# Performance work log

Hardware: AMD Instinct MI355X
Metric: run time of the kernel (lower is better)

Reference implementation:

```python
import jax, jax.numpy as jnp
import numpy as np

B, S, D, H = 2, 2048, 1024, 16
DK = D // H


def setup_inputs() -> dict:
    key = jax.random.key(0)
    ks = jax.random.split(key, 13)
    std = 1.0 / np.sqrt(D)
    inp = {
        "query": jax.random.normal(ks[0], (B, S, D), jnp.float32),
        "key": jax.random.normal(ks[1], (B, S, D), jnp.float32),
        "value": jax.random.normal(ks[2], (B, S, D), jnp.float32),
        "mask": jax.random.randint(ks[3], (B, S, S), 0, 2, jnp.int32),
        "Wq": jax.random.normal(ks[4], (D, D), jnp.float32) * std,
        "bq": jax.random.normal(ks[5], (D,), jnp.float32) * std,
        "Wk": jax.random.normal(ks[6], (D, D), jnp.float32) * std,
        "bk": jax.random.normal(ks[7], (D,), jnp.float32) * std,
        "Wv": jax.random.normal(ks[8], (D, D), jnp.float32) * std,
        "bv": jax.random.normal(ks[9], (D,), jnp.float32) * std,
        "Wo": jax.random.normal(ks[10], (D, D), jnp.float32) * std,
        "bo": jax.random.normal(ks[11], (D,), jnp.float32) * std,
    }
    return inp


def reference(query, key, value, mask, Wq, bq, Wk, bk, Wv, bv, Wo, bo):
    # QKV projections (torch Linear: x @ W.T + b), then split heads -> [B,H,S,DK]
    def proj(x, W, b):
        return (x @ W.T + b).reshape(B, S, H, DK).transpose(0, 2, 1, 3)

    q = proj(query, Wq, bq)
    k = proj(key, Wk, bk)
    v = proj(value, Wv, bv)

    scores = jnp.einsum("bhqd,bhkd->bhqk", q, k) / np.sqrt(DK)
    # mask [B,S,S] broadcast over heads; masked_fill(mask==0, -1e9)
    scores = jnp.where(mask[:, None, :, :] == 0, jnp.float32(-1e9), scores)
    p_attn = jax.nn.softmax(scores, axis=-1)
    x = jnp.einsum("bhqk,bhkd->bhqd", p_attn, v)
    x = x.transpose(0, 2, 1, 3).reshape(B, S, D)
    return x @ Wo.T + bo
```

## Files before the change

### kernel.cpp

```cpp
#include <hip/hip_runtime.h>
#include <hip/hip_bf16.h>
#include <cstdint>
#include <cstddef>

#define NB 2
#define NS 2048
#define ND 1024
#define NH 16
#define NDK 64
#define NT (NS / 64)

typedef __attribute__((ext_vector_type(4))) float f32x4;
typedef __attribute__((ext_vector_type(8))) short bf16x8;

#define MFMA_16x16x32_BF16(a,b,c) __builtin_amdgcn_mfma_f32_16x16x32_bf16((a),(b),(c),0,0,0)

__device__ __forceinline__ uint16_t f2bf(float f){
  uint32_t u = __float_as_uint(f);
  u += 0x7fffu + ((u >> 16) & 1u);
  return (uint16_t)(u >> 16);
}
__device__ __forceinline__ uint32_t bfpack2(float a, float b){
  uint32_t r;
  asm volatile("v_cvt_pk_bf16_f32 %0, %1, %2" : "=v"(r) : "v"(a), "v"(b));
  return r;
}
__device__ __forceinline__ void gload_lds16(const void* g, void* l){
  __builtin_amdgcn_global_load_lds((const __attribute__((address_space(1))) void*)g,
                                   (__attribute__((address_space(3))) void*)l, 16, 0, 0);
}

__global__ void prep_inputs(const float* __restrict__ a, const float* __restrict__ b2,
                            const float* __restrict__ c, uint16_t* __restrict__ oa,
                            uint16_t* __restrict__ ob, uint16_t* __restrict__ oc,
                            const int* __restrict__ mask, unsigned long long* __restrict__ bits,
                            int n8, int nchunks){
  if(blockIdx.y == 3){
    int wid  = (blockIdx.x * blockDim.x + threadIdx.x) >> 6;
    int lane = threadIdx.x & 63;
    int nw   = (gridDim.x * blockDim.x) >> 6;
    for(int ch = wid; ch < nchunks; ch += nw){
      int mv = mask[(size_t)ch * 64 + lane];
      unsigned long long bb = __ballot(mv != 0);
      if(lane == 0) bits[ch] = bb;
    }
    return;
  }
  const float* in = (blockIdx.y == 0) ? a : (blockIdx.y == 1) ? b2 : c;
  uint16_t* out   = (blockIdx.y == 0) ? oa : (blockIdx.y == 1) ? ob : oc;
  int i0 = blockIdx.x * blockDim.x + threadIdx.x;
  int stride = gridDim.x * blockDim.x;
  for(int i = i0; i < n8; i += stride){
    const float4* p = (const float4*)(in) + (size_t)i * 2;
    float4 x = p[0], y = p[1];
    bf16x8 o;
    o[0]=(short)f2bf(x.x); o[1]=(short)f2bf(x.y); o[2]=(short)f2bf(x.z); o[3]=(short)f2bf(x.w);
    o[4]=(short)f2bf(y.x); o[5]=(short)f2bf(y.y); o[6]=(short)f2bf(y.z); o[7]=(short)f2bf(y.w);
    *((bf16x8*)(out) + i) = o;
  }
}
__global__ void cvt4_f32_bf16(const float* __restrict__ a, const float* __restrict__ b2,
                              const float* __restrict__ c, const float* __restrict__ d,
                              uint16_t* __restrict__ oa, uint16_t* __restrict__ ob,
                              uint16_t* __restrict__ oc, uint16_t* __restrict__ od, int n8){
  const float* in = (blockIdx.y == 0) ? a : (blockIdx.y == 1) ? b2 : (blockIdx.y == 2) ? c : d;
  uint16_t* out   = (blockIdx.y == 0) ? oa : (blockIdx.y == 1) ? ob : (blockIdx.y == 2) ? oc : od;
  int i0 = blockIdx.x * blockDim.x + threadIdx.x;
  int stride = gridDim.x * blockDim.x;
  for(int i = i0; i < n8; i += stride){
    const float4* p = (const float4*)(in) + (size_t)i * 2;
    float4 x = p[0], y = p[1];
    bf16x8 o;
    o[0]=(short)f2bf(x.x); o[1]=(short)f2bf(x.y); o[2]=(short)f2bf(x.z); o[3]=(short)f2bf(x.w);
    o[4]=(short)f2bf(y.x); o[5]=(short)f2bf(y.y); o[6]=(short)f2bf(y.z); o[7]=(short)f2bf(y.w);
    *((bf16x8*)(out) + i) = o;
  }
}

template<bool OUTF32>
__global__ __launch_bounds__(256, 4)
void gemm_bt(const uint16_t* __restrict__ A0, const uint16_t* __restrict__ A1, const uint16_t* __restrict__ A2,
             const uint16_t* __restrict__ W0, const uint16_t* __restrict__ W1, const uint16_t* __restrict__ W2,
             const float* __restrict__ b0, const float* __restrict__ b1, const float* __restrict__ b2,
             void* __restrict__ C0, void* __restrict__ C1, void* __restrict__ C2,
             int M, int N, int K, int vtz)
{
  const int z = blockIdx.z;
  const uint16_t* A   = (z == 0) ? A0 : (z == 1) ? A1 : A2;
  const uint16_t* W   = (z == 0) ? W0 : (z == 1) ? W1 : W2;
  const float*   bias = (z == 0) ? b0 : (z == 1) ? b1 : b2;
  void*          Cout = (z == 0) ? C0 : (z == 1) ? C1 : C2;

  __shared__ __align__(16) uint16_t Asm[128 * 64];
  __shared__ __align__(16) uint16_t Bsm[128 * 64];

  const int t = threadIdx.x;
  const int lane = t & 63, w = t >> 6;
  const int l15 = lane & 15, g = lane >> 4;
  const int bm = blockIdx.y * 128, bn = blockIdx.x * 128;
  const int wr = (w >> 1) * 64, wc = (w & 1) * 64;

  f32x4 acc[4][4] = {};

  const int srow = lane >> 3;
  const int schk = (lane & 7) ^ srow;

  const uint16_t* gA = A + (size_t)(bm + w * 32 + srow) * K + schk * 8;
  const uint16_t* gB = W + (size_t)(bn + w * 32 + srow) * K + schk * 8;
  uint16_t* lA = &Asm[(w * 32) * 64];
  uint16_t* lB = &Bsm[(w * 32) * 64];

  const int xr = l15 & 7;
  int aOff[2][4], bOff[2][4];
  #pragma unroll
  for(int kk = 0; kk < 2; ++kk)
    #pragma unroll
    for(int m = 0; m < 4; ++m){
      aOff[kk][m] = (wr + m*16 + l15) * 64 + (((kk*4 + g) ^ xr) << 3);
      bOff[kk][m] = (wc + m*16 + l15) * 64 + (((kk*4 + g) ^ xr) << 3);
    }

  for(int k0 = 0; k0 < K; k0 += 64){
    #pragma unroll
    for(int j = 0; j < 4; ++j){
      gload_lds16(gA + (size_t)(8 * j) * K, lA + (8 * j) * 64);
      gload_lds16(gB + (size_t)(8 * j) * K, lB + (8 * j) * 64);
    }
    gA += 64; gB += 64;
    __syncthreads();
    #pragma unroll
    for(int kk = 0; kk < 2; ++kk){
      bf16x8 af[4], bfr[4];
      #pragma unroll
      for(int m = 0; m < 4; ++m) af[m]  = *(const bf16x8*)&Asm[aOff[kk][m]];
      #pragma unroll
      for(int n = 0; n < 4; ++n) bfr[n] = *(const bf16x8*)&Bsm[bOff[kk][n]];
      #pragma unroll
      for(int m = 0; m < 4; ++m)
        #pragma unroll
        for(int n = 0; n < 4; ++n)
          acc[m][n] = MFMA_16x16x32_BF16(af[m], bfr[n], acc[m][n]);
    }
    __syncthreads();
  }

  if(z == vtz){
    uint16_t* Vt = (uint16_t*)Cout;
    #pragma unroll
    for(int m = 0; m < 4; ++m){
      const int row = bm + wr + m*16 + g*4;
      const int bb = row >> 11, ss = row & (NS - 1);
      #pragma unroll
      for(int n = 0; n < 4; ++n){
        const int col = bn + wc + n*16 + l15;
        const float bv = bias[col];
        float v0 = acc[m][n][0] + bv, v1 = acc[m][n][1] + bv;
        float v2 = acc[m][n][2] + bv, v3 = acc[m][n][3] + bv;
        uint2 pk; pk.x = bfpack2(v0, v1); pk.y = bfpack2(v2, v3);
        size_t dst = ((size_t)(bb * NH + (col >> 6)) * NDK + (col & 63)) * NS + ss;
        *(uint2*)&Vt[dst] = pk;
      }
    }
  } else {
    #pragma unroll
    for(int m = 0; m < 4; ++m){
      const int row = bm + wr + m*16 + g*4;
      #pragma unroll
      for(int n = 0; n < 4; ++n){
        const int col = bn + wc + n*16 + l15;
        const float bv = bias[col];
        #pragma unroll
        for(int j = 0; j < 4; ++j){
          float v = acc[m][n][j] + bv;
          if (OUTF32) ((float*)Cout)[(size_t)(row + j) * N + col] = v;
          else        ((uint16_t*)Cout)[(size_t)(row + j) * N + col] = f2bf(v);
        }
      }
    }
  }
}

__device__ __forceinline__ int swz64(int r, int chunk){
  return r * 64 + (((chunk) ^ (r & 7)) << 3);
}

__global__ __launch_bounds__(256, 4)
void attn_fwd(const uint16_t* __restrict__ Qp, const uint16_t* __restrict__ Kp,
              const uint16_t* __restrict__ Vtg, const uint2* __restrict__ Mbits,
              uint16_t* __restrict__ Xo)
{
  __shared__ __align__(16) uint16_t Ksm[2][64 * 64];
  __shared__ __align__(16) uint16_t Vtsm[2][64 * 64];
  __shared__ __align__(16) uint16_t Psm[4][16 * 64];

  const int t = threadIdx.x, lane = t & 63, w = t >> 6;
  const int l15 = lane & 15, g = lane >> 4;
  const int b = blockIdx.z, h = blockIdx.y, q0 = blockIdx.x * 64;
  const int qbase = q0 + w * 16;

  bf16x8 qf0, qf1;
  {
    const uint16_t* qptr = Qp + (size_t)(b * NS + qbase + l15) * ND + h * NDK + g * 8;
    qf0 = *(const bf16x8*)(qptr);
    qf1 = *(const bf16x8*)(qptr + 32);
  }

  bf16x8 ones;
  #pragma unroll
  for(int e = 0; e < 8; ++e) ones[e] = (short)0x3F80;

  f32x4 acc[4] = {};
  f32x4 acl = {};
  const float SCL = 0.125f * 1.44269504f;
  const float MC  = 23.0831f;

  const int srow = lane >> 3;
  const int schk = (lane & 7) ^ srow;

  const uint16_t* gK0 = Kp + (size_t)(b * NS + w * 16 + srow) * ND + h * NDK + schk * 8;
  const uint16_t* gK1 = gK0 + 8 * ND;
  const uint16_t* gV0 = Vtg + (size_t)(b * NH + h) * NDK * NS + (size_t)(w * 16 + srow) * NS + schk * 8;
  const uint16_t* gV1 = gV0 + 8 * NS;

  uint16_t* lK = &Ksm[0][(w * 16) * 64];
  uint16_t* lV = &Vtsm[0][(w * 16) * 64];

  int kOffA[4], kOffB[4], vOff[2][4];
  #pragma unroll
  for(int i = 0; i < 4; ++i){
    kOffA[i] = swz64(i * 16 + l15, g);
    kOffB[i] = swz64(i * 16 + l15, g + 4);
  }
  #pragma unroll
  for(int c2 = 0; c2 < 2; ++c2)
    #pragma unroll
    for(int tt = 0; tt < 4; ++tt)
      vOff[c2][tt] = swz64(tt * 16 + l15, c2 * 4 + g);
  const int xorw = (l15 & 7) << 3;
  const int prow = l15 * 64;
  int pW[4], pR[2];
  #pragma unroll
  for(int i = 0; i < 4; ++i) pW[i] = prow + ((16 * i + g * 4) ^ xorw);
  #pragma unroll
  for(int c2 = 0; c2 < 2; ++c2) pR[c2] = prow + ((c2 * 32 + g * 8) ^ xorw);
  uint16_t* PsmW = Psm[w];

  const uint2* Mptr = Mbits + (size_t)(b * NS + qbase + l15) * (NS / 64);

  gload_lds16(gK0, lK);
  gload_lds16(gK1, lK + 8 * 64);
  gload_lds16(gV0, lV);
  gload_lds16(gV1, lV + 8 * 64);
  uint2 mmc = Mptr[0];
  gK0 += 64 * ND; gK1 += 64 * ND; gV0 += 64; gV1 += 64;

  int cur = 0;
  for(int ti = 0; ti < NT; ++ti){
    uint2 mmn;
    if(ti + 1 < NT){
      const int nc = (cur ^ 1) * 4096;
      gload_lds16(gK0, lK + nc);
      gload_lds16(gK1, lK + nc + 8 * 64);
      gload_lds16(gV0, lV + nc);
      gload_lds16(gV1, lV + nc + 8 * 64);
      mmn = Mptr[ti + 1];
      gK0 += 64 * ND; gK1 += 64 * ND; gV0 += 64; gV1 += 64;
      asm volatile("s_waitcnt vmcnt(5)" ::: "memory");
    } else {
      asm volatile("s_waitcnt vmcnt(0)" ::: "memory");
    }
    __builtin_amdgcn_s_barrier();

    const uint16_t* Kc = &Ksm[0][cur * 4096];
    const uint16_t* Vc = &Vtsm[0][cur * 4096];

    f32x4 s4[4];
    __builtin_amdgcn_s_setprio(1);
    #pragma unroll
    for(int i = 0; i < 4; ++i){
      bf16x8 kf0 = *(const bf16x8*)&Kc[kOffA[i]];
      bf16x8 kf1 = *(const bf16x8*)&Kc[kOffB[i]];
      f32x4 zr = {};
      zr = MFMA_16x16x32_BF16(kf0, qf0, zr);
      zr = MFMA_16x16x32_BF16(kf1, qf1, zr);
      s4[i] = zr;
    }
    __builtin_amdgcn_s_setprio(0);

    const uint32_t w0 = mmc.x >> (g * 4);
    const uint32_t w1 = mmc.y >> (g * 4);
    #pragma unroll
    for(int i = 0; i < 4; ++i){
      const uint32_t ww = (i < 2) ? w0 : w1;
      #pragma unroll
      for(int j = 0; j < 4; ++j){
        const int bitpos = (i & 1) * 16 + j;
        float e = exp2f(fmaf(s4[i][j], SCL, -MC));
        uint32_t sm = (uint32_t)(((int)(ww << (31 - bitpos))) >> 31);
        s4[i][j] = __uint_as_float(sm & __float_as_uint(e));
      }
    }

    #pragma unroll
    for(int i = 0; i < 4; ++i){
      uint2 pk;
      pk.x = bfpack2(s4[i][0], s4[i][1]);
      pk.y = bfpack2(s4[i][2], s4[i][3]);
      *(uint2*)&PsmW[pW[i]] = pk;
    }

    __builtin_amdgcn_s_setprio(1);
    #pragma unroll
    for(int c2 = 0; c2 < 2; ++c2){
      bf16x8 pf = *(const bf16x8*)&PsmW[pR[c2]];
      acl = MFMA_16x16x32_BF16(pf, ones, acl);
      #pragma unroll
      for(int tt = 0; tt < 4; ++tt){
        bf16x8 vf = *(const bf16x8*)&Vc[vOff[c2][tt]];
        acc[tt] = MFMA_16x16x32_BF16(pf, vf, acc[tt]);
      }
    }
    __builtin_amdgcn_s_setprio(0);

    asm volatile("s_waitcnt lgkmcnt(0)" ::: "memory");
    __builtin_amdgcn_s_barrier();
    cur ^= 1;
    mmc = mmn;
  }

  #pragma unroll
  for(int j = 0; j < 4; ++j){
    const float inv = 1.0f / acl[j];
    const int qr = qbase + g * 4 + j;
    #pragma unroll
    for(int tt = 0; tt < 4; ++tt)
      Xo[(size_t)(b * NS + qr) * ND + h * NDK + tt * 16 + l15] = f2bf(acc[tt][j] * inv);
  }
}

extern "C" void kernel_launch(void* const* d_in, const int* in_sizes, int n_in,
                              void* d_out, int out_size, void* d_ws, size_t ws_size,
                              hipStream_t stream)
{
  const float* query = (const float*)d_in[0];
  const float* key   = (const float*)d_in[1];
  const float* value = (const float*)d_in[2];
  const int*   mask  = (const int*)d_in[3];
  const float* Wq = (const float*)d_in[4];
  const float* bq = (const float*)d_in[5];
  const float* Wk = (const float*)d_in[6];
  const float* bk = (const float*)d_in[7];
  const float* Wv = (const float*)d_in[8];
  const float* bv = (const float*)d_in[9];
  const float* Wo = (const float*)d_in[10];
  const float* bo = (const float*)d_in[11];
  float* out = (float*)d_out;

  const size_t NX = (size_t)NB * NS * ND;
  const size_t NW = (size_t)ND * ND;

  uint16_t* ws  = (uint16_t*)d_ws;
  uint16_t* Xq  = ws;
  uint16_t* Xk  = Xq  + NX;
  uint16_t* Xv  = Xk  + NX;
  uint16_t* Wqb = Xv  + NX;
  uint16_t* Wkb = Wqb + NW;
  uint16_t* Wvb = Wkb + NW;
  uint16_t* Wob = Wvb + NW;
  uint16_t* Qp  = Wob + NW;
  uint16_t* Kp  = Qp  + NX;
  uint16_t* Vt  = Kp  + NX;
  uint16_t* Xa  = Vt  + NX;
  unsigned long long* Mb = (unsigned long long*)(Xa + NX);

  const int nchunks = (int)((size_t)NB * NS * NS / 64);

  prep_inputs<<<dim3(2048, 4), 256, 0, stream>>>(query, key, value, Xq, Xk, Xv,
                                                 mask, Mb, (int)(NX / 8), nchunks);
  cvt4_f32_bf16<<<dim3(512, 4), 256, 0, stream>>>(Wq, Wk, Wv, Wo, Wqb, Wkb, Wvb, Wob, (int)(NW / 8));

  dim3 gproj(ND / 128, (NB * NS) / 128, 3);
  gemm_bt<false><<<gproj, 256, 0, stream>>>(Xq, Xk, Xv,
                                            Wqb, Wkb, Wvb,
                                            bq, bk, bv,
                                            (void*)Qp, (void*)Kp, (void*)Vt,
                                            NB * NS, ND, ND, 2);

  attn_fwd<<<dim3(NS / 64, NH, NB), 256, 0, stream>>>(Qp, Kp, Vt, (const uint2*)Mb, Xa);

  dim3 gout(ND / 128, (NB * NS) / 128, 1);
  gemm_bt<true><<<gout, 256, 0, stream>>>(Xa, Xa, Xa,
                                          Wob, Wob, Wob,
                                          bo, bo, bo,
                                          (void*)out, (void*)out, (void*)out,
                                          NB * NS, ND, ND, -1);
}
```

Baseline: 160.8 us.

## Double-buffer GEMM LDS tiles and merge conversion kernels into one launch

The projection and output GEMMs now use two LDS buffers per operand and issue the global-to-LDS loads for the next K tile before computing on the current one. Explicit vmcnt waits and raw barriers replace __syncthreads, so memory latency can overlap with MFMA work. The separate activation and weight conversion kernels are also merged into a single launch that handles all seven tensors plus the mask bit packing. The cost is doubled LDS per GEMM block, which may reduce occupancy under the 4-blocks-per-CU launch bound.

```diff
diff --git a/kernel.cpp b/kernel.cpp
--- a/kernel.cpp
+++ b/kernel.cpp
@@ -30,12 +30,18 @@
                                    (__attribute__((address_space(3))) void*)l, 16, 0, 0);
 }
 
-__global__ void prep_inputs(const float* __restrict__ a, const float* __restrict__ b2,
-                            const float* __restrict__ c, uint16_t* __restrict__ oa,
-                            uint16_t* __restrict__ ob, uint16_t* __restrict__ oc,
-                            const int* __restrict__ mask, unsigned long long* __restrict__ bits,
-                            int n8, int nchunks){
-  if(blockIdx.y == 3){
+__global__ void prep_all(const float* __restrict__ q, const float* __restrict__ k,
+                         const float* __restrict__ v,
+                         const float* __restrict__ wq, const float* __restrict__ wk,
+                         const float* __restrict__ wv, const float* __restrict__ wo,
+                         uint16_t* __restrict__ oq, uint16_t* __restrict__ ok,
+                         uint16_t* __restrict__ ov,
+                         uint16_t* __restrict__ owq, uint16_t* __restrict__ owk,
+                         uint16_t* __restrict__ owv, uint16_t* __restrict__ owo,
+                         const int* __restrict__ mask, unsigned long long* __restrict__ bits,
+                         int n8a, int n8w, int nchunks){
+  const int y = blockIdx.y;
+  if(y == 3){
     int wid  = (blockIdx.x * blockDim.x + threadIdx.x) >> 6;
     int lane = threadIdx.x & 63;
     int nw   = (gridDim.x * blockDim.x) >> 6;
@@ -46,33 +52,24 @@
     }
     return;
   }
-  const float* in = (blockIdx.y == 0) ? a : (blockIdx.y == 1) ? b2 : c;
-  uint16_t* out   = (blockIdx.y == 0) ? oa : (blockIdx.y == 1) ? ob : oc;
+  const float* in; uint16_t* out; int n8;
+  switch(y){
+    case 0: in = q;  out = oq;  n8 = n8a; break;
+    case 1: in = k;  out = ok;  n8 = n8a; break;
+    case 2: in = v;  out = ov;  n8 = n8a; break;
+    case 4: in = wq; out = owq; n8 = n8w; break;
+    case 5: in = wk; out = owk; n8 = n8w; break;
+    case 6: in = wv; out = owv; n8 = n8w; break;
+    default: in = wo; out = owo; n8 = n8w; break;
+  }
   int i0 = blockIdx.x * blockDim.x + threadIdx.x;
   int stride = gridDim.x * blockDim.x;
   for(int i = i0; i < n8; i += stride){
     const float4* p = (const float4*)(in) + (size_t)i * 2;
-    float4 x = p[0], y = p[1];
+    float4 x = p[0], yv = p[1];
     bf16x8 o;
-    o[0]=(short)f2bf(x.x); o[1]=(short)f2bf(x.y); o[2]=(short)f2bf(x.z); o[3]=(short)f2bf(x.w);
-    o[4]=(short)f2bf(y.x); o[5]=(short)f2bf(y.y); o[6]=(short)f2bf(y.z); o[7]=(short)f2bf(y.w);
-    *((bf16x8*)(out) + i) = o;
-  }
-}
-__global__ void cvt4_f32_bf16(const float* __restrict__ a, const float* __restrict__ b2,
-                              const float* __restrict__ c, const float* __restrict__ d,
-                              uint16_t* __restrict__ oa, uint16_t* __restrict__ ob,
-                              uint16_t* __restrict__ oc, uint16_t* __restrict__ od, int n8){
-  const float* in = (blockIdx.y == 0) ? a : (blockIdx.y == 1) ? b2 : (blockIdx.y == 2) ? c : d;
-  uint16_t* out   = (blockIdx.y == 0) ? oa : (blockIdx.y == 1) ? ob : (blockIdx.y == 2) ? oc : od;
-  int i0 = blockIdx.x * blockDim.x + threadIdx.x;
-  int stride = gridDim.x * blockDim.x;
-  for(int i = i0; i < n8; i += stride){
-    const float4* p = (const float4*)(in) + (size_t)i * 2;
-    float4 x = p[0], y = p[1];
-    bf16x8 o;
-    o[0]=(short)f2bf(x.x); o[1]=(short)f2bf(x.y); o[2]=(short)f2bf(x.z); o[3]=(short)f2bf(x.w);
-    o[4]=(short)f2bf(y.x); o[5]=(short)f2bf(y.y); o[6]=(short)f2bf(y.z); o[7]=(short)f2bf(y.w);
+    o[0]=(short)f2bf(x.x);  o[1]=(short)f2bf(x.y);  o[2]=(short)f2bf(x.z);  o[3]=(short)f2bf(x.w);
+    o[4]=(short)f2bf(yv.x); o[5]=(short)f2bf(yv.y); o[6]=(short)f2bf(yv.z); o[7]=(short)f2bf(yv.w);
     *((bf16x8*)(out) + i) = o;
   }
 }
@@ -91,8 +88,8 @@
   const float*   bias = (z == 0) ? b0 : (z == 1) ? b1 : b2;
   void*          Cout = (z == 0) ? C0 : (z == 1) ? C1 : C2;
 
-  __shared__ __align__(16) uint16_t Asm[128 * 64];
-  __shared__ __align__(16) uint16_t Bsm[128 * 64];
+  __shared__ __align__(16) uint16_t Asm[2][128 * 64];
+  __shared__ __align__(16) uint16_t Bsm[2][128 * 64];
 
   const int t = threadIdx.x;
   const int lane = t & 63, w = t >> 6;
@@ -107,8 +104,8 @@
 
   const uint16_t* gA = A + (size_t)(bm + w * 32 + srow) * K + schk * 8;
   const uint16_t* gB = W + (size_t)(bn + w * 32 + srow) * K + schk * 8;
-  uint16_t* lA = &Asm[(w * 32) * 64];
-  uint16_t* lB = &Bsm[(w * 32) * 64];
+  uint16_t* lA = &Asm[0][(w * 32) * 64];
+  uint16_t* lB = &Bsm[0][(w * 32) * 64];
 
   const int xr = l15 & 7;
   int aOff[2][4], bOff[2][4];
@@ -120,28 +117,48 @@
       bOff[kk][m] = (wc + m*16 + l15) * 64 + (((kk*4 + g) ^ xr) << 3);
     }
 
-  for(int k0 = 0; k0 < K; k0 += 64){
-    #pragma unroll
-    for(int j = 0; j < 4; ++j){
-      gload_lds16(gA + (size_t)(8 * j) * K, lA + (8 * j) * 64);
-      gload_lds16(gB + (size_t)(8 * j) * K, lB + (8 * j) * 64);
-    }
-    gA += 64; gB += 64;
-    __syncthreads();
+  #pragma unroll
+  for(int j = 0; j < 4; ++j){
+    gload_lds16(gA + (size_t)(8 * j) * K, lA + (8 * j) * 64);
+    gload_lds16(gB + (size_t)(8 * j) * K, lB + (8 * j) * 64);
+  }
+  gA += 64; gB += 64;
+
+  const int NIT = K >> 6;
+  int cur = 0;
+  for(int ti = 0; ti < NIT; ++ti){
+    if(ti + 1 < NIT){
+      const int nb = (cur ^ 1) * (128 * 64);
+      #pragma unroll
+      for(int j = 0; j < 4; ++j){
+        gload_lds16(gA + (size_t)(8 * j) * K, lA + nb + (8 * j) * 64);
+        gload_lds16(gB + (size_t)(8 * j) * K, lB + nb + (8 * j) * 64);
+      }
+      gA += 64; gB += 64;
+      asm volatile("s_waitcnt vmcnt(8)" ::: "memory");
+    } else {
+      asm volatile("s_waitcnt vmcnt(0)" ::: "memory");
+    }
+    __builtin_amdgcn_s_barrier();
+
+    const uint16_t* As = &Asm[0][0] + cur * (128 * 64);
+    const uint16_t* Bs = &Bsm[0][0] + cur * (128 * 64);
     #pragma unroll
     for(int kk = 0; kk < 2; ++kk){
       bf16x8 af[4], bfr[4];
       #pragma unroll
-      for(int m = 0; m < 4; ++m) af[m]  = *(const bf16x8*)&Asm[aOff[kk][m]];
-      #pragma unroll
-      for(int n = 0; n < 4; ++n) bfr[n] = *(const bf16x8*)&Bsm[bOff[kk][n]];
+      for(int m = 0; m < 4; ++m) af[m]  = *(const bf16x8*)&As[aOff[kk][m]];
+      #pragma unroll
+      for(int n = 0; n < 4; ++n) bfr[n] = *(const bf16x8*)&Bs[bOff[kk][n]];
       #pragma unroll
       for(int m = 0; m < 4; ++m)
         #pragma unroll
         for(int n = 0; n < 4; ++n)
           acc[m][n] = MFMA_16x16x32_BF16(af[m], bfr[n], acc[m][n]);
     }
-    __syncthreads();
+    asm volatile("s_waitcnt lgkmcnt(0)" ::: "memory");
+    __builtin_amdgcn_s_barrier();
+    cur ^= 1;
   }
 
   if(z == vtz){
@@ -375,9 +392,9 @@
 
   const int nchunks = (int)((size_t)NB * NS * NS / 64);
 
-  prep_inputs<<<dim3(2048, 4), 256, 0, stream>>>(query, key, value, Xq, Xk, Xv,
-                                                 mask, Mb, (int)(NX / 8), nchunks);
-  cvt4_f32_bf16<<<dim3(512, 4), 256, 0, stream>>>(Wq, Wk, Wv, Wo, Wqb, Wkb, Wvb, Wob, (int)(NW / 8));
+  prep_all<<<dim3(1024, 8), 256, 0, stream>>>(query, key, value, Wq, Wk, Wv, Wo,
+                                              Xq, Xk, Xv, Wqb, Wkb, Wvb, Wob,
+                                              mask, Mb, (int)(NX / 8), (int)(NW / 8), nchunks);
 
   dim3 gproj(ND / 128, (NB * NS) / 128, 3);
   gemm_bt<false><<<gproj, 256, 0, stream>>>(Xq, Xk, Xv,
```

After: 168.8 us. 5.0% more time.
